# Kernel tuning notes

Hardware: AMD Instinct MI355X
Metric: run time of the kernel (lower is better)

## Reference

```python
import jax, jax.numpy as jnp
import numpy as np

FG_FRACTION = 0.25
FG_THRESH = 0.5
BG_HI = 0.5
BG_LO = 0.1
BATCHSIZE = 256
FG_ROIS_PER_IMAGE = int(round(FG_FRACTION * BATCHSIZE))  # 64


def _iou(a, b):
    # a: [N,4], b: [K,4]; keras_rcnn overlap uses the +1 pixel convention
    ax1, ay1, ax2, ay2 = a[:, 0:1], a[:, 1:2], a[:, 2:3], a[:, 3:4]
    bx1, by1, bx2, by2 = b[:, 0], b[:, 1], b[:, 2], b[:, 3]
    iw = jnp.maximum(jnp.minimum(ax2, bx2) - jnp.maximum(ax1, bx1) + 1.0, 0.0)
    ih = jnp.maximum(jnp.minimum(ay2, by2) - jnp.maximum(ay1, by1) + 1.0, 0.0)
    inter = iw * ih  # [N,K]
    area_a = (ax2 - ax1 + 1.0) * (ay2 - ay1 + 1.0)  # [N,1]
    area_b = (bx2 - bx1 + 1.0) * (by2 - by1 + 1.0)  # [K]
    return inter / (area_a + area_b - inter)


def _bbox_transform(ex, gt):
    ew = ex[:, 2] - ex[:, 0] + 1.0
    eh = ex[:, 3] - ex[:, 1] + 1.0
    ecx = ex[:, 0] + 0.5 * ew
    ecy = ex[:, 1] + 0.5 * eh
    gw = gt[:, 2] - gt[:, 0] + 1.0
    gh = gt[:, 3] - gt[:, 1] + 1.0
    gcx = gt[:, 0] + 0.5 * gw
    gcy = gt[:, 1] + 0.5 * gh
    tx = (gcx - ecx) / ew
    ty = (gcy - ecy) / eh
    tw = jnp.log(gw / ew)
    th = jnp.log(gh / eh)
    return jnp.stack([tx, ty, tw, th], axis=1)


def _random_boxes(key, n, img=1000.0):
    k1, k2, k3, k4 = jax.random.split(key, 4)
    cx = jax.random.uniform(k1, (n,)) * (img - 200.0) + 100.0
    cy = jax.random.uniform(k2, (n,)) * (img - 200.0) + 100.0
    w = jax.random.uniform(k3, (n,)) * 150.0 + 30.0
    h = jax.random.uniform(k4, (n,)) * 150.0 + 30.0
    return jnp.stack([cx - 0.5 * w, cy - 0.5 * h, cx + 0.5 * w, cy + 0.5 * h], axis=1)


def setup_inputs() -> dict:
    key = jax.random.key(0)
    N, K, C = 50000, 500, 81
    kg, kl, kj, kr = jax.random.split(key, 4)
    gt = _random_boxes(kg, K)
    labels_int = jax.random.randint(kl, (K,), 1, C)
    gt_labels = jax.nn.one_hot(labels_int, C, dtype=jnp.float32)
    # 10*K jittered copies of gt boxes -> guaranteed fg pool; rest random -> bg pool
    reps = 10
    fg_props = jnp.tile(gt, (reps, 1)) + jax.random.normal(kj, (reps * K, 4)) * 3.0
    rand_props = _random_boxes(kr, N - reps * K)
    proposals = jnp.concatenate([fg_props, rand_props], axis=0)[None]  # [1,N,4]
    return {"proposals": proposals, "gt_labels": gt_labels[None], "gt_boxes": gt[None]}


def _proposal_target(proposals, gt_labels, gt_boxes):
    p = proposals[0]
    g = gt_boxes[0].astype(jnp.float32)
    lab1h = gt_labels[0]
    num_classes = lab1h.shape[1]

    all_rois = jnp.concatenate([p, g], axis=0)  # [N+K,4]
    n_total = all_rois.shape[0]

    gt_cls = jnp.argmax(lab1h, axis=1)                 # [K]
    overlaps = _iou(all_rois, g)                       # [N+K,K]
    gt_assignment = jnp.argmax(overlaps, axis=1)       # [N+K]
    max_overlaps = jnp.max(overlaps, axis=1)           # [N+K]
    labels_all = gt_cls[gt_assignment]                 # [N+K]

    fg_mask = max_overlaps >= FG_THRESH
    bg_mask = (max_overlaps < BG_HI) & (max_overlaps >= BG_LO)

    order = jnp.arange(n_total)
    # stable: fg/bg indices first (in index order), others pushed to the back
    fg_sorted = jnp.argsort(jnp.where(fg_mask, order, order + n_total))
    bg_sorted = jnp.argsort(jnp.where(bg_mask, order, order + n_total))

    n_fg = jnp.sum(fg_mask)
    n_bg = jnp.sum(bg_mask)
    fg_count = jnp.minimum(FG_ROIS_PER_IMAGE, n_fg)
    bg_count = jnp.minimum(BATCHSIZE - fg_count, n_bg)

    slots = jnp.arange(BATCHSIZE)
    is_fg_slot = slots < fg_count
    keep = jnp.where(
        is_fg_slot,
        fg_sorted[jnp.clip(slots, 0, n_total - 1)],
        bg_sorted[jnp.clip(slots - fg_count, 0, n_total - 1)],
    )
    valid = slots < (fg_count + bg_count)

    rois = all_rois[keep]                                   # [256,4]
    labels_kept = jnp.where(is_fg_slot & valid, labels_all[keep], 0)  # bg -> 0
    gt_kept = g[gt_assignment[keep]]                        # [256,4]

    targets = _bbox_transform(rois, gt_kept)                # [256,4]
    oh = jax.nn.one_hot(labels_kept, num_classes, dtype=jnp.float32)
    pos = (labels_kept > 0).astype(jnp.float32)
    # expand to 4K form: only the assigned class gets nonzero targets
    bbox_targets = (oh * pos[:, None])[:, :, None] * targets[:, None, :]
    bbox_targets = bbox_targets.reshape(BATCHSIZE, 4 * num_classes)

    labels_out = oh  # one_hot of (fg labels, 0 for bg)
    return rois[None], labels_out[None], bbox_targets[None]


def reference(proposals, gt_labels, gt_boxes):
    return _proposal_target(proposals, gt_labels, gt_boxes)
```

## Files before the change

### kernel.cpp

```cpp
#include <hip/hip_runtime.h>

#define BATCH   256
#define FG_CAP  64
#define BG_CAP  192
#define NB_CAP  256
#define SPLIT   8
#define ROIS_PB 32

__device__ __forceinline__ void iou_id(const float4 a, float area_a,
                                       const float4 g, float area_g,
                                       float& inter, float& denom)
{
    float iw = fmaxf(__fadd_rn(__fsub_rn(fminf(a.z, g.z), fmaxf(a.x, g.x)), 1.0f), 0.0f);
    float ih = fmaxf(__fadd_rn(__fsub_rn(fminf(a.w, g.w), fmaxf(a.y, g.y)), 1.0f), 0.0f);
    inter = __fmul_rn(iw, ih);
    denom = __fsub_rn(__fadd_rn(area_a, area_g), inter);
}

__global__ __launch_bounds__(256) void pt_classify(
    const float* __restrict__ props, const float* __restrict__ gtb,
    const float* __restrict__ gtl,
    int* __restrict__ packed, int* __restrict__ gtcls,
    int n_prop, int K, int C, int n_total, int roi_blocks)
{
    if ((int)blockIdx.x >= roi_blocks) {
        int t = ((int)blockIdx.x - roi_blocks) * 256 + (int)threadIdx.x;
        if (t < K) {
            const float* row = gtl + (size_t)t * C;
            float best = row[0]; int bc = 0;
            for (int c = 1; c < C; ++c) {
                float v = row[c];
                if (v > best) { best = v; bc = c; }
            }
            gtcls[t] = bc;
        }
        return;
    }

    __shared__ float4 s_gt[512];
    __shared__ float  s_area[512];
    for (int k = threadIdx.x; k < K; k += 256) {
        float x1 = gtb[4*k+0], y1 = gtb[4*k+1], x2 = gtb[4*k+2], y2 = gtb[4*k+3];
        s_gt[k] = make_float4(x1, y1, x2, y2);
        s_area[k] = __fmul_rn(__fadd_rn(__fsub_rn(x2, x1), 1.0f),
                              __fadd_rn(__fsub_rn(y2, y1), 1.0f));
    }
    __syncthreads();

    int i     = (int)blockIdx.x * ROIS_PB + (int)threadIdx.x / SPLIT;
    int slice = (int)threadIdx.x & (SPLIT - 1);
    if (i >= n_total) return;

    float4 a = (i < n_prop) ? ((const float4*)props)[i]
                            : ((const float4*)gtb)[i - n_prop];
    float area_a = __fmul_rn(__fadd_rn(__fsub_rn(a.z, a.x), 1.0f),
                             __fadd_rn(__fsub_rn(a.w, a.y), 1.0f));

    float bi = -1.0f, bd = 1.0f; int bk = 0x7FFFFFFF;
    int k = slice;
    for (; k + 3 * SPLIT < K; k += 4 * SPLIT) {
        float4 g0 = s_gt[k];            float q0 = s_area[k];
        float4 g1 = s_gt[k +   SPLIT];  float q1 = s_area[k +   SPLIT];
        float4 g2 = s_gt[k + 2*SPLIT];  float q2 = s_area[k + 2*SPLIT];
        float4 g3 = s_gt[k + 3*SPLIT];  float q3 = s_area[k + 3*SPLIT];
        float i0,d0,i1,d1,i2,d2,i3,d3;
        iou_id(a, area_a, g0, q0, i0, d0);
        iou_id(a, area_a, g1, q1, i1, d1);
        iou_id(a, area_a, g2, q2, i2, d2);
        iou_id(a, area_a, g3, q3, i3, d3);
        float iA, dA; int kA;
        if (i1 * d0 > i0 * d1) { iA = i1; dA = d1; kA = k + SPLIT; }
        else                   { iA = i0; dA = d0; kA = k; }
        float iB, dB; int kB;
        if (i3 * d2 > i2 * d3) { iB = i3; dB = d3; kB = k + 3*SPLIT; }
        else                   { iB = i2; dB = d2; kB = k + 2*SPLIT; }
        if (iB * dA > iA * dB) { iA = iB; dA = dB; kA = kB; }
        if (iA * bd > bi * dA) { bi = iA; bd = dA; bk = kA; }
    }
    for (; k < K; k += SPLIT) {
        float4 g = s_gt[k]; float q = s_area[k];
        float in_, dn;
        iou_id(a, area_a, g, q, in_, dn);
        if (in_ * bd > bi * dn) { bi = in_; bd = dn; bk = k; }
    }

    #pragma unroll
    for (int m = 1; m < SPLIT; m <<= 1) {
        float oi = __shfl_xor(bi, m, 64);
        float od = __shfl_xor(bd, m, 64);
        int   ok = __shfl_xor(bk, m, 64);
        float lhs = oi * bd, rhs = bi * od;
        if (lhs > rhs || (lhs == rhs && ok < bk)) { bi = oi; bd = od; bk = ok; }
    }

    if (slice == 0) {
        float iou = __fdiv_rn(bi, bd);
        int cls = 0;
        if (iou >= 0.5f)      cls = 1;
        else if (iou >= 0.1f) cls = 2;
        packed[i] = bk | (cls << 16);
    }
}

__global__ __launch_bounds__(1024) void pt_compact(
    const int* __restrict__ packed,
    int* __restrict__ fg_list, int* __restrict__ bg_list,
    int* __restrict__ nb_list, int* __restrict__ counts, int n_total)
{
    __shared__ int w_f[16], w_b[16], w_n[16];
    __shared__ int s_run[3], s_stop;
    const int tid = (int)threadIdx.x;
    if (tid == 0) { s_run[0] = 0; s_run[1] = 0; s_run[2] = 0; s_stop = 0; }
    __syncthreads();

    const int lane = tid & 63, wave = tid >> 6;
    const unsigned long long ltm = (1ull << lane) - 1ull;

    for (int base = 0; base < n_total; base += 8192) {
        int idx0 = base + tid * 8;
        int code = 0;
        if (idx0 + 7 < n_total) {
            int4 p0 = ((const int4*)packed)[idx0 >> 2];
            int4 p1 = ((const int4*)packed)[(idx0 >> 2) + 1];
            code  = (p0.x >> 16)        | ((p0.y >> 16) << 2)
                  | ((p0.z >> 16) << 4) | ((p0.w >> 16) << 6)
                  | ((p1.x >> 16) << 8) | ((p1.y >> 16) << 10)
                  | ((p1.z >> 16) << 12)| ((p1.w >> 16) << 14);
        } else {
            #pragma unroll
            for (int j = 0; j < 8; ++j) {
                int c = (idx0 + j < n_total) ? (packed[idx0 + j] >> 16) : 3;
                code |= c << (2 * j);
            }
        }

        int eF = 0, eB = 0, eN = 0, tF = 0, tB = 0, tN = 0;
        #pragma unroll
        for (int j = 0; j < 8; ++j) {
            int c = (code >> (2 * j)) & 3;
            unsigned long long bF = __ballot(c == 1);
            unsigned long long bB = __ballot(c == 2);
            unsigned long long bN = __ballot(c == 0 || c == 1);
            eF += (int)__popcll(bF & ltm); tF += (int)__popcll(bF);
            eB += (int)__popcll(bB & ltm); tB += (int)__popcll(bB);
            eN += (int)__popcll(bN & ltm); tN += (int)__popcll(bN);
        }
        if (lane == 0) { w_f[wave] = tF; w_b[wave] = tB; w_n[wave] = tN; }
        int r0 = s_run[0], r1 = s_run[1], r2 = s_run[2];
        __syncthreads();

        int pf = 0, pb = 0, pn = 0;
        for (int w = 0; w < wave; ++w) { pf += w_f[w]; pb += w_b[w]; pn += w_n[w]; }
        int rF = r0 + pf + eF, rB = r1 + pb + eB, rN = r2 + pn + eN;
        #pragma unroll
        for (int j = 0; j < 8; ++j) {
            int c = (code >> (2 * j)) & 3;
            int idx = idx0 + j;
            if (c == 1)           { if (rF < FG_CAP) fg_list[rF] = idx; rF++; }
            if (c == 2)           { if (rB < BG_CAP) bg_list[rB] = idx; rB++; }
            if (c == 0 || c == 1) { if (rN < NB_CAP) nb_list[rN] = idx; rN++; }
        }
        if (tid == 0) {
            int sf = 0, sb = 0, sn = 0;
            for (int w = 0; w < 16; ++w) { sf += w_f[w]; sb += w_b[w]; sn += w_n[w]; }
            s_run[0] += sf; s_run[1] += sb; s_run[2] += sn;
            if (s_run[0] >= FG_CAP && s_run[1] >= BG_CAP) s_stop = 1;
        }
        __syncthreads();
        if (s_stop) break;
    }
    if (tid == 0) { counts[0] = s_run[0]; counts[1] = s_run[1]; counts[2] = s_run[2]; }
}

__global__ __launch_bounds__(128) void pt_output(
    const float* __restrict__ props, const float* __restrict__ gtb,
    const int* __restrict__ packed, const int* __restrict__ gtcls,
    const int* __restrict__ fg_list, const int* __restrict__ bg_list,
    const int* __restrict__ nb_list, const int* __restrict__ counts,
    float* __restrict__ out, int n_prop, int K, int C)
{
    __shared__ float sh[8];
    __shared__ int   sh_label;
    int s = blockIdx.x;

    if (threadIdx.x == 0) {
        int fg_total = counts[0], bg_total = counts[1];
        int fg_count = min(FG_CAP, fg_total);
        bool is_fg = (s < fg_count);
        int keep;
        if (is_fg) keep = fg_list[s];
        else { int j = s - fg_count; keep = (j < bg_total) ? bg_list[j] : nb_list[j - bg_total]; }
        int pk = packed[keep];
        int assign = pk & 0xFFFF;
        int label = is_fg ? gtcls[assign] : 0;

        float4 roi = (keep < n_prop) ? ((const float4*)props)[keep]
                                     : ((const float4*)gtb)[keep - n_prop];
        float4 g = ((const float4*)gtb)[assign];

        float ew  = roi.z - roi.x + 1.0f;
        float eh  = roi.w - roi.y + 1.0f;
        float ecx = roi.x + 0.5f * ew;
        float ecy = roi.y + 0.5f * eh;
        float gw  = g.z - g.x + 1.0f;
        float gh  = g.w - g.y + 1.0f;
        float gcx = g.x + 0.5f * gw;
        float gcy = g.y + 0.5f * gh;
        sh[0] = roi.x; sh[1] = roi.y; sh[2] = roi.z; sh[3] = roi.w;
        sh[4] = (gcx - ecx) / ew;
        sh[5] = (gcy - ecy) / eh;
        sh[6] = logf(gw / ew);
        sh[7] = logf(gh / eh);
        sh_label = label;
    }
    __syncthreads();

    int label = sh_label;

    if (threadIdx.x < 4) out[s * 4 + threadIdx.x] = sh[threadIdx.x];

    float* outl = out + 4 * BATCH;
    for (int c = threadIdx.x; c < C; c += 128)
        outl[s * C + c] = (c == label) ? 1.0f : 0.0f;

    float4* outb = (float4*)(out + 4 * BATCH + (size_t)BATCH * C) + (size_t)s * C;
    float4 tv = make_float4(sh[4], sh[5], sh[6], sh[7]);
    float4 zv = make_float4(0.f, 0.f, 0.f, 0.f);
    for (int c = threadIdx.x; c < C; c += 128)
        outb[c] = (label > 0 && c == label) ? tv : zv;
}

extern "C" void kernel_launch(void* const* d_in, const int* in_sizes, int n_in,
                              void* d_out, int out_size, void* d_ws, size_t ws_size,
                              hipStream_t stream)
{
    const float* props = (const float*)d_in[0];
    const float* gtl   = (const float*)d_in[1];
    const float* gtb   = (const float*)d_in[2];
    float* out = (float*)d_out;

    int n_prop  = in_sizes[0] / 4;
    int K       = in_sizes[2] / 4;
    int C       = in_sizes[1] / K;
    int n_total = n_prop + K;

    int* ws_packed = (int*)d_ws;
    int* ws_gtcls  = ws_packed + ((n_total + 3) & ~3);
    int* ws_fg     = ws_gtcls + ((K + 3) & ~3);
    int* ws_bg     = ws_fg + FG_CAP;
    int* ws_nb     = ws_bg + BG_CAP;
    int* ws_cnt    = ws_nb + NB_CAP;

    int roi_blocks = (n_total + ROIS_PB - 1) / ROIS_PB;
    int gt_blocks  = (K + 255) / 256;

    pt_classify<<<roi_blocks + gt_blocks, 256, 0, stream>>>(
        props, gtb, gtl, ws_packed, ws_gtcls, n_prop, K, C, n_total, roi_blocks);
    pt_compact<<<1, 1024, 0, stream>>>(
        ws_packed, ws_fg, ws_bg, ws_nb, ws_cnt, n_total);
    pt_output<<<BATCH, 128, 0, stream>>>(
        props, gtb, ws_packed, ws_gtcls, ws_fg, ws_bg, ws_nb, ws_cnt,
        out, n_prop, K, C);
}
```

Before: 88.44 us.

## Fuse compaction and output into one kernel with in-block gt argmax

The compaction and output kernels are merged into a single 1024-thread block. It keeps the fg, bg and fallback index lists in shared memory and writes all 256 output rows directly, with four threads per row. The separate gt-label argmax pass in the classify kernel is removed; the argmax is done only for the foreground slots inside the finish kernel, using a shuffle reduction. This saves one launch and the global-memory round trips for the lists and counts. In exchange, all output writes now come from one CU instead of 256 blocks.

```diff
diff --git a/kernel.cpp b/kernel.cpp
--- a/kernel.cpp
+++ b/kernel.cpp
@@ -19,24 +19,9 @@
 
 __global__ __launch_bounds__(256) void pt_classify(
     const float* __restrict__ props, const float* __restrict__ gtb,
-    const float* __restrict__ gtl,
-    int* __restrict__ packed, int* __restrict__ gtcls,
-    int n_prop, int K, int C, int n_total, int roi_blocks)
-{
-    if ((int)blockIdx.x >= roi_blocks) {
-        int t = ((int)blockIdx.x - roi_blocks) * 256 + (int)threadIdx.x;
-        if (t < K) {
-            const float* row = gtl + (size_t)t * C;
-            float best = row[0]; int bc = 0;
-            for (int c = 1; c < C; ++c) {
-                float v = row[c];
-                if (v > best) { best = v; bc = c; }
-            }
-            gtcls[t] = bc;
-        }
-        return;
-    }
-
+    int* __restrict__ packed,
+    int n_prop, int K, int n_total)
+{
     __shared__ float4 s_gt[512];
     __shared__ float  s_area[512];
     for (int k = threadIdx.x; k < K; k += 256) {
@@ -102,11 +87,13 @@
     }
 }
 
-__global__ __launch_bounds__(1024) void pt_compact(
+__global__ __launch_bounds__(1024) void pt_finish(
+    const float* __restrict__ props, const float* __restrict__ gtb,
+    const float* __restrict__ gtl,
     const int* __restrict__ packed,
-    int* __restrict__ fg_list, int* __restrict__ bg_list,
-    int* __restrict__ nb_list, int* __restrict__ counts, int n_total)
-{
+    float* __restrict__ out, int n_prop, int K, int C, int n_total)
+{
+    __shared__ int l_fg[FG_CAP], l_bg[BG_CAP], l_nb[NB_CAP];
     __shared__ int w_f[16], w_b[16], w_n[16];
     __shared__ int s_run[3], s_stop;
     const int tid = (int)threadIdx.x;
@@ -156,9 +143,9 @@
         for (int j = 0; j < 8; ++j) {
             int c = (code >> (2 * j)) & 3;
             int idx = idx0 + j;
-            if (c == 1)           { if (rF < FG_CAP) fg_list[rF] = idx; rF++; }
-            if (c == 2)           { if (rB < BG_CAP) bg_list[rB] = idx; rB++; }
-            if (c == 0 || c == 1) { if (rN < NB_CAP) nb_list[rN] = idx; rN++; }
+            if (c == 1)           { if (rF < FG_CAP) l_fg[rF] = idx; rF++; }
+            if (c == 2)           { if (rB < BG_CAP) l_bg[rB] = idx; rB++; }
+            if (c == 0 || c == 1) { if (rN < NB_CAP) l_nb[rN] = idx; rN++; }
         }
         if (tid == 0) {
             int sf = 0, sb = 0, sn = 0;
@@ -169,64 +156,60 @@
         __syncthreads();
         if (s_stop) break;
     }
-    if (tid == 0) { counts[0] = s_run[0]; counts[1] = s_run[1]; counts[2] = s_run[2]; }
-}
-
-__global__ __launch_bounds__(128) void pt_output(
-    const float* __restrict__ props, const float* __restrict__ gtb,
-    const int* __restrict__ packed, const int* __restrict__ gtcls,
-    const int* __restrict__ fg_list, const int* __restrict__ bg_list,
-    const int* __restrict__ nb_list, const int* __restrict__ counts,
-    float* __restrict__ out, int n_prop, int K, int C)
-{
-    __shared__ float sh[8];
-    __shared__ int   sh_label;
-    int s = blockIdx.x;
-
-    if (threadIdx.x == 0) {
-        int fg_total = counts[0], bg_total = counts[1];
-        int fg_count = min(FG_CAP, fg_total);
-        bool is_fg = (s < fg_count);
-        int keep;
-        if (is_fg) keep = fg_list[s];
-        else { int j = s - fg_count; keep = (j < bg_total) ? bg_list[j] : nb_list[j - bg_total]; }
-        int pk = packed[keep];
-        int assign = pk & 0xFFFF;
-        int label = is_fg ? gtcls[assign] : 0;
-
-        float4 roi = (keep < n_prop) ? ((const float4*)props)[keep]
-                                     : ((const float4*)gtb)[keep - n_prop];
-        float4 g = ((const float4*)gtb)[assign];
-
-        float ew  = roi.z - roi.x + 1.0f;
-        float eh  = roi.w - roi.y + 1.0f;
-        float ecx = roi.x + 0.5f * ew;
-        float ecy = roi.y + 0.5f * eh;
-        float gw  = g.z - g.x + 1.0f;
-        float gh  = g.w - g.y + 1.0f;
-        float gcx = g.x + 0.5f * gw;
-        float gcy = g.y + 0.5f * gh;
-        sh[0] = roi.x; sh[1] = roi.y; sh[2] = roi.z; sh[3] = roi.w;
-        sh[4] = (gcx - ecx) / ew;
-        sh[5] = (gcy - ecy) / eh;
-        sh[6] = logf(gw / ew);
-        sh[7] = logf(gh / eh);
-        sh_label = label;
-    }
-    __syncthreads();
-
-    int label = sh_label;
-
-    if (threadIdx.x < 4) out[s * 4 + threadIdx.x] = sh[threadIdx.x];
-
-    float* outl = out + 4 * BATCH;
-    for (int c = threadIdx.x; c < C; c += 128)
-        outl[s * C + c] = (c == label) ? 1.0f : 0.0f;
+
+    int fgt = s_run[0], bgt = s_run[1];
+    int fg_count = min(FG_CAP, fgt);
+    int s   = tid >> 2;
+    int sub = tid & 3;
+    bool is_fg = (s < fg_count);
+    int keep;
+    if (is_fg) keep = l_fg[s];
+    else { int j = s - fg_count; keep = (j < bgt) ? l_bg[j] : l_nb[j - bgt]; }
+
+    int assign = packed[keep] & 0xFFFF;
+
+    int label = 0;
+    if (is_fg) {
+        const float* row = gtl + (size_t)assign * C;
+        int st = sub * 21, en = min(C, st + 21);
+        float bv = -1.0f; int bc = 0x7FFF;
+        for (int c = st; c < en; ++c) {
+            float v = row[c];
+            if (v > bv) { bv = v; bc = c; }
+        }
+        #pragma unroll
+        for (int m = 1; m < 4; m <<= 1) {
+            float ov = __shfl_xor(bv, m, 64);
+            int   oc = __shfl_xor(bc, m, 64);
+            if (ov > bv || (ov == bv && oc < bc)) { bv = ov; bc = oc; }
+        }
+        label = bc;
+    }
+
+    float4 roi = (keep < n_prop) ? ((const float4*)props)[keep]
+                                 : ((const float4*)gtb)[keep - n_prop];
+    float4 g = ((const float4*)gtb)[assign];
+
+    float ew  = roi.z - roi.x + 1.0f;
+    float eh  = roi.w - roi.y + 1.0f;
+    float ecx = roi.x + 0.5f * ew;
+    float ecy = roi.y + 0.5f * eh;
+    float gw  = g.z - g.x + 1.0f;
+    float gh  = g.w - g.y + 1.0f;
+    float gcx = g.x + 0.5f * gw;
+    float gcy = g.y + 0.5f * gh;
+    float4 tv = make_float4((gcx - ecx) / ew, (gcy - ecy) / eh,
+                            logf(gw / ew), logf(gh / eh));
+    float4 zv = make_float4(0.f, 0.f, 0.f, 0.f);
+
+    if (sub == 0) ((float4*)out)[s] = roi;
+
+    float* outl = out + 4 * BATCH + (size_t)s * C;
+    for (int c = sub; c < C; c += 4)
+        outl[c] = (c == label) ? 1.0f : 0.0f;
 
     float4* outb = (float4*)(out + 4 * BATCH + (size_t)BATCH * C) + (size_t)s * C;
-    float4 tv = make_float4(sh[4], sh[5], sh[6], sh[7]);
-    float4 zv = make_float4(0.f, 0.f, 0.f, 0.f);
-    for (int c = threadIdx.x; c < C; c += 128)
+    for (int c = sub; c < C; c += 4)
         outb[c] = (label > 0 && c == label) ? tv : zv;
 }
 
@@ -245,20 +228,11 @@
     int n_total = n_prop + K;
 
     int* ws_packed = (int*)d_ws;
-    int* ws_gtcls  = ws_packed + ((n_total + 3) & ~3);
-    int* ws_fg     = ws_gtcls + ((K + 3) & ~3);
-    int* ws_bg     = ws_fg + FG_CAP;
-    int* ws_nb     = ws_bg + BG_CAP;
-    int* ws_cnt    = ws_nb + NB_CAP;
 
     int roi_blocks = (n_total + ROIS_PB - 1) / ROIS_PB;
-    int gt_blocks  = (K + 255) / 256;
-
-    pt_classify<<<roi_blocks + gt_blocks, 256, 0, stream>>>(
-        props, gtb, gtl, ws_packed, ws_gtcls, n_prop, K, C, n_total, roi_blocks);
-    pt_compact<<<1, 1024, 0, stream>>>(
-        ws_packed, ws_fg, ws_bg, ws_nb, ws_cnt, n_total);
-    pt_output<<<BATCH, 128, 0, stream>>>(
-        props, gtb, ws_packed, ws_gtcls, ws_fg, ws_bg, ws_nb, ws_cnt,
-        out, n_prop, K, C);
-}
+
+    pt_classify<<<roi_blocks, 256, 0, stream>>>(
+        props, gtb, ws_packed, n_prop, K, n_total);
+    pt_finish<<<1, 1024, 0, stream>>>(
+        props, gtb, gtl, ws_packed, out, n_prop, K, C, n_total);
+}
```

Result: slower. 99.61 us (+12.6%).
